# Optimization experiments

Hardware: AMD Instinct MI355X
Metric: run time of the kernel (lower is better)

Reference implementation:

```python
import jax, jax.numpy as jnp
import numpy as np

N_EMBD = 1024
N_HEAD = 16
LORA_R = 8
LORA_ALPHA = 16
SCALE = LORA_ALPHA / LORA_R


def lora_linear(x, W, b, A, Bm):
    # loralib: F.linear(x, W, b) + (x @ A.T @ B.T) * scaling
    return x @ W.T + b + ((x @ A.T) @ Bm.T) * SCALE


def setup_inputs() -> dict:
    key = jax.random.key(0)
    ks = jax.random.split(key, 9)
    B, T, C = 4, 2048, N_EMBD
    s_in = 1.0 / np.sqrt(C)
    x = jax.random.normal(ks[0], (B, T, C), dtype=jnp.float32)
    Wqkv = jax.random.normal(ks[1], (3 * C, C), dtype=jnp.float32) * s_in
    bqkv = jnp.zeros((3 * C,), dtype=jnp.float32)
    Aqkv = jax.random.normal(ks[2], (LORA_R, C), dtype=jnp.float32) * s_in
    Bqkv = jnp.zeros((3 * C, LORA_R), dtype=jnp.float32)  # loralib inits B to zero
    Wproj = jax.random.normal(ks[3], (C, C), dtype=jnp.float32) * s_in
    bproj = jnp.zeros((C,), dtype=jnp.float32)
    Aproj = jax.random.normal(ks[4], (LORA_R, C), dtype=jnp.float32) * s_in
    Bproj = jnp.zeros((C, LORA_R), dtype=jnp.float32)
    return {"x": x, "Wqkv": Wqkv, "bqkv": bqkv, "Aqkv": Aqkv, "Bqkv": Bqkv,
            "Wproj": Wproj, "bproj": bproj, "Aproj": Aproj, "Bproj": Bproj}


def reference(x, Wqkv, bqkv, Aqkv, Bqkv, Wproj, bproj, Aproj, Bproj):
    B, T, C = x.shape
    H, D = N_HEAD, C // N_HEAD
    qkv = lora_linear(x, Wqkv, bqkv, Aqkv, Bqkv)  # [B,T,3C]
    q, k, v = jnp.split(qkv, 3, axis=2)
    # [B,T,C] -> [B,H,T,D]
    q = q.reshape(B, T, H, D).transpose(0, 2, 1, 3)
    k = k.reshape(B, T, H, D).transpose(0, 2, 1, 3)
    v = v.reshape(B, T, H, D).transpose(0, 2, 1, 3)
    att = jnp.einsum("bhqd,bhkd->bhqk", q, k) * (1.0 / np.sqrt(D))
    causal = jnp.tril(jnp.ones((T, T), dtype=bool))
    att = jnp.where(causal[None, None], att, jnp.float32(-jnp.inf))
    att = jax.nn.softmax(att, axis=-1)
    out = jnp.einsum("bhqk,bhkd->bhqd", att, v)  # [B,H,T,D]
    out = out.transpose(0, 2, 1, 3).reshape(B, T, C)
    return lora_linear(out, Wproj, bproj, Aproj, Bproj)
```

## Files before the change

### kernel.cpp

```cpp
#include <hip/hip_runtime.h>
#include <hip/hip_bf16.h>

typedef __bf16 bf16_t;
typedef __bf16 bf16x8 __attribute__((ext_vector_type(8)));
typedef __bf16 bf16x4 __attribute__((ext_vector_type(4)));
typedef float  f32x4  __attribute__((ext_vector_type(4)));

#define MFMA_BF16 __builtin_amdgcn_mfma_f32_16x16x32_bf16
#define NEG_BIG  (-3.0e38f)

#if __has_builtin(__builtin_amdgcn_exp2f)
#define EXP2F(x) __builtin_amdgcn_exp2f(x)
#else
#define EXP2F(x) exp2f(x)
#endif

#define SBAR()       __builtin_amdgcn_s_barrier()
#define SCHED0()     __builtin_amdgcn_sched_barrier(0)
#define WAIT_LGKM0() asm volatile("s_waitcnt lgkmcnt(0)" ::: "memory")
#define WAIT_LGKM8() asm volatile("s_waitcnt lgkmcnt(8)" ::: "memory")
#define WAIT_VM0()   asm volatile("s_waitcnt vmcnt(0)" ::: "memory")
#define WAIT_VM4()   asm volatile("s_waitcnt vmcnt(4)" ::: "memory")
#define WAIT_VM6()   asm volatile("s_waitcnt vmcnt(6)" ::: "memory")

__device__ __forceinline__ void load16_lds(const bf16_t* g, bf16_t* l) {
    __builtin_amdgcn_global_load_lds(
        (const __attribute__((address_space(1))) void*)g,
        (__attribute__((address_space(3))) void*)l, 16, 0, 0);
}

__device__ inline bf16x8 ld8(const bf16_t* p) { return *(const bf16x8*)p; }
__device__ inline bf16x8 ld8(const float* p) {
    f32x4 a = *(const f32x4*)p;
    f32x4 b = *(const f32x4*)(p + 4);
    bf16x8 o;
    o[0] = (bf16_t)a[0]; o[1] = (bf16_t)a[1]; o[2] = (bf16_t)a[2]; o[3] = (bf16_t)a[3];
    o[4] = (bf16_t)b[0]; o[5] = (bf16_t)b[1]; o[6] = (bf16_t)b[2]; o[7] = (bf16_t)b[3];
    return o;
}

template <typename TX>
__device__ __forceinline__ void lora_xa_body(
    const TX* __restrict__ X, const float* __restrict__ A,
    float* __restrict__ out, int m, int lane)
{
    const TX* xp = X + (size_t)m * 1024;
    float acc[8];
#pragma unroll
    for (int r = 0; r < 8; r++) acc[r] = 0.f;

#pragma unroll 4
    for (int ci = 0; ci < 16; ci++) {
        int k = ci * 64 + lane;
        float xv = (float)xp[k];
#pragma unroll
        for (int r = 0; r < 8; r++) acc[r] += xv * A[r * 1024 + k];
    }
#pragma unroll
    for (int r = 0; r < 8; r++) {
        float v = acc[r];
        v += __shfl_xor(v, 1);  v += __shfl_xor(v, 2);  v += __shfl_xor(v, 4);
        v += __shfl_xor(v, 8);  v += __shfl_xor(v, 16); v += __shfl_xor(v, 32);
        if (lane == 0) out[m * 8 + r] = v;
    }
}

template <typename TX>
__global__ __launch_bounds__(256) void lora_xa_kernel(
    const TX* __restrict__ X, const float* __restrict__ A,
    float* __restrict__ out)
{
    const int lane = threadIdx.x & 63;
    const int w    = threadIdx.x >> 6;
    const int m    = blockIdx.x * 4 + w;
    lora_xa_body<TX>(X, A, out, m, lane);
}

__global__ __launch_bounds__(256) void prep_kernel(
    const float* __restrict__ x, const float* __restrict__ Wqkv,
    const float* __restrict__ Wproj,
    bf16_t* __restrict__ x16, bf16_t* __restrict__ Wqkv16,
    bf16_t* __restrict__ Wproj16,
    const float* __restrict__ Aqkv, float* __restrict__ xa1)
{
    const int bid = blockIdx.x;
    if (bid < 6144) {
        const float* in; bf16_t* out; size_t off;
        if (bid < 4096)      { in = x;     out = x16;     off = (size_t)bid * 2048; }
        else if (bid < 5632) { in = Wqkv;  out = Wqkv16;  off = (size_t)(bid - 4096) * 2048; }
        else                 { in = Wproj; out = Wproj16; off = (size_t)(bid - 5632) * 2048; }
        size_t i = off + (size_t)threadIdx.x * 8;
        *(bf16x8*)&out[i] = ld8(&in[i]);
    } else {
        const int lane = threadIdx.x & 63;
        const int w    = threadIdx.x >> 6;
        const int m    = (bid - 6144) * 4 + w;
        lora_xa_body<float>(x, Aqkv, xa1, m, lane);
    }
}

__device__ __forceinline__ void gemm_epilogue(
    f32x4 (&acc)[4][4], const float* bias, const float* xA, const float* LB,
    bf16_t* C0, bf16_t* C1, bf16_t* C2, float* Cf,
    int tile_m, int tile_n, int wm, int wn, int c, int g)
{
    const int seg    = tile_n >> 10;
    const int tn_loc = tile_n & 1023;
    bf16_t* Cout = (seg == 0) ? C0 : (seg == 1) ? C1 : C2;

    float biasf[4];
    float lbv[4][8];
#pragma unroll
    for (int j = 0; j < 4; j++) {
        int col = tile_n + wn + j * 16 + c;
        biasf[j] = bias[col];
        f32x4 lb0 = *(const f32x4*)&LB[(size_t)col * 8];
        f32x4 lb1 = *(const f32x4*)&LB[(size_t)col * 8 + 4];
#pragma unroll
        for (int r = 0; r < 4; r++) { lbv[j][r] = lb0[r]; lbv[j][r + 4] = lb1[r]; }
    }
#pragma unroll
    for (int i = 0; i < 4; i++) {
#pragma unroll
        for (int rg = 0; rg < 4; rg++) {
            int row = tile_m + wm + i * 16 + g * 4 + rg;
            f32x4 xa0 = *(const f32x4*)&xA[(size_t)row * 8];
            f32x4 xa1 = *(const f32x4*)&xA[(size_t)row * 8 + 4];
#pragma unroll
            for (int j = 0; j < 4; j++) {
                float lora = xa0[0] * lbv[j][0] + xa0[1] * lbv[j][1] +
                             xa0[2] * lbv[j][2] + xa0[3] * lbv[j][3] +
                             xa1[0] * lbv[j][4] + xa1[1] * lbv[j][5] +
                             xa1[2] * lbv[j][6] + xa1[3] * lbv[j][7];
                float v = acc[i][j][rg] + biasf[j] + 2.0f * lora;
                int lcol = tn_loc + wn + j * 16 + c;
                if (Cf) Cf[(size_t)row * 1024 + lcol] = v;
                else    Cout[(size_t)row * 1024 + lcol] = (bf16_t)v;
            }
        }
    }
}

template <typename TA, typename TW>
__global__ __launch_bounds__(256) void gemm_bias_lora(
    const TA* __restrict__ A, const TW* __restrict__ W,
    const float* __restrict__ bias, const float* __restrict__ xA,
    const float* __restrict__ LB,
    bf16_t* __restrict__ C0, bf16_t* __restrict__ C1, bf16_t* __restrict__ C2,
    float* __restrict__ Cf, int K)
{
    __shared__ __align__(16) bf16_t As[128 * 72];
    __shared__ __align__(16) bf16_t Bs[128 * 72];

    const int t    = threadIdx.x;
    const int lane = t & 63;
    const int w    = t >> 6;
    const int wm   = (w >> 1) * 64;
    const int wn   = (w & 1) * 64;
    const int c    = lane & 15;
    const int g    = lane >> 4;
    const int tile_m = blockIdx.y * 128;
    const int tile_n = blockIdx.x * 128;

    const int srow = t >> 3;
    const int scol = (t & 7) * 8;

    f32x4 acc[4][4];
#pragma unroll
    for (int i = 0; i < 4; i++)
#pragma unroll
        for (int j = 0; j < 4; j++) {
            f32x4 z = {0.f, 0.f, 0.f, 0.f};
            acc[i][j] = z;
        }

    for (int k0 = 0; k0 < K; k0 += 64) {
#pragma unroll
        for (int i = 0; i < 4; i++) {
            int r = srow + i * 32;
            *(bf16x8*)&As[r * 72 + scol] = ld8(&A[(size_t)(tile_m + r) * K + k0 + scol]);
            *(bf16x8*)&Bs[r * 72 + scol] = ld8(&W[(size_t)(tile_n + r) * K + k0 + scol]);
        }
        __syncthreads();

#pragma unroll
        for (int kk = 0; kk < 2; kk++) {
            bf16x8 af[4], bfr[4];
#pragma unroll
            for (int i = 0; i < 4; i++)
                af[i] = *(const bf16x8*)&As[(wm + i * 16 + c) * 72 + kk * 32 + g * 8];
#pragma unroll
            for (int j = 0; j < 4; j++)
                bfr[j] = *(const bf16x8*)&Bs[(wn + j * 16 + c) * 72 + kk * 32 + g * 8];
#pragma unroll
            for (int i = 0; i < 4; i++)
#pragma unroll
                for (int j = 0; j < 4; j++)
                    acc[i][j] = MFMA_BF16(af[i], bfr[j], acc[i][j], 0, 0, 0);
        }
        __syncthreads();
    }
    gemm_epilogue(acc, bias, xA, LB, C0, C1, C2, Cf, tile_m, tile_n, wm, wn, c, g);
}

__global__ __launch_bounds__(512, 2) void gemm_256(
    const bf16_t* __restrict__ A, const bf16_t* __restrict__ W,
    const float* __restrict__ bias, const float* __restrict__ xA,
    const float* __restrict__ LB,
    bf16_t* __restrict__ C0, bf16_t* __restrict__ C1, bf16_t* __restrict__ C2,
    float* __restrict__ Cf, int K, int ntn)
{
    __shared__ __align__(16) bf16_t As[4][8192];
    __shared__ __align__(16) bf16_t Bs[4][8192];

    const int t    = threadIdx.x;
    const int lane = t & 63;
    const int w    = t >> 6;
    const int c    = lane & 15;
    const int g    = lane >> 4;

    const int nwg = gridDim.x;
    const int cpx = nwg >> 3;
    const int bid = blockIdx.x;
    const int swz = (bid & 7) * cpx + (bid >> 3);
    const int tile_m = (swz / ntn) * 256;
    const int tile_n = (swz % ntn) * 256;

    const int wm  = (w >> 2) * 128;
    const int wn  = (w & 3) * 64;
    const int ha  = w >> 2;
    const int hb  = wn >> 7;
    const int wnl = wn & 127;

    int aoffs[8][2], boffs[4][2];
#pragma unroll
    for (int il = 0; il < 8; il++) {
        int rl = il * 16 + c;
#pragma unroll
        for (int ks = 0; ks < 2; ks++)
            aoffs[il][ks] = rl * 64 + (((ks * 4 + g) ^ (rl & 7)) * 8);
    }
#pragma unroll
    for (int j2 = 0; j2 < 4; j2++) {
        int rl = wnl + j2 * 16 + c;
#pragma unroll
        for (int ks = 0; ks < 2; ks++)
            boffs[j2][ks] = rl * 64 + (((ks * 4 + g) ^ (rl & 7)) * 8);
    }

    const int trow = t >> 3;
    const int qq   = (t & 7) ^ (trow & 7);
    const bf16_t* aO = A + (size_t)(tile_m + trow) * K + qq * 8;
    const bf16_t* wO = W + (size_t)(tile_n + trow) * K + qq * 8;
    const size_t rK64 = (size_t)64 * K;

#define STAGE_A(T, h) do {                                                         \
    load16_lds(aO + (size_t)(h) * 128 * K + (size_t)(T) * 64,                      \
               &As[((T) & 1) * 2 + (h)][t * 8]);                                   \
    load16_lds(aO + (size_t)(h) * 128 * K + rK64 + (size_t)(T) * 64,               \
               &As[((T) & 1) * 2 + (h)][4096 + t * 8]); } while (0)
#define STAGE_B(T, h) do {                                                         \
    load16_lds(wO + (size_t)(h) * 128 * K + (size_t)(T) * 64,                      \
               &Bs[((T) & 1) * 2 + (h)][t * 8]);                                   \
    load16_lds(wO + (size_t)(h) * 128 * K + rK64 + (size_t)(T) * 64,               \
               &Bs[((T) & 1) * 2 + (h)][4096 + t * 8]); } while (0)

    f32x4 acc[8][4];
#pragma unroll
    for (int i = 0; i < 8; i++)
#pragma unroll
        for (int j2 = 0; j2 < 4; j2++) {
            f32x4 z = {0.f, 0.f, 0.f, 0.f};
            acc[i][j2] = z;
        }

    const int NT = K >> 6;

    STAGE_B(0, 0); STAGE_B(0, 1); STAGE_A(0, 0); STAGE_A(0, 1);
    WAIT_VM4();
    STAGE_B(1, 0); STAGE_B(1, 1); STAGE_A(1, 0);
    WAIT_VM6();
    SBAR();

    for (int j = 0; j < NT; j++) {
        const bf16_t* Ab = &As[(j & 1) * 2 + ha][0];
        const bf16_t* Bb = &Bs[(j & 1) * 2 + hb][0];
        bf16x8 bfr[4][2], af0[4], af1[4];

#pragma unroll
        for (int j2 = 0; j2 < 4; j2++) {
            bfr[j2][0] = *(const bf16x8*)&Bb[boffs[j2][0]];
            bfr[j2][1] = *(const bf16x8*)&Bb[boffs[j2][1]];
        }
#pragma unroll
        for (int i = 0; i < 4; i++) af0[i] = *(const bf16x8*)&Ab[aoffs[i][0]];
        if (j + 1 < NT) STAGE_A(j + 1, 1);
        WAIT_LGKM8();
        SBAR();
        WAIT_LGKM0();
        SCHED0();
        __builtin_amdgcn_s_setprio(1);
#pragma unroll
        for (int i = 0; i < 4; i++)
#pragma unroll
            for (int j2 = 0; j2 < 4; j2++)
                acc[i][j2] = MFMA_BF16(af0[i], bfr[j2][0], acc[i][j2], 0, 0, 0);
        __builtin_amdgcn_s_setprio(0);
        SBAR();

#pragma unroll
        for (int i = 0; i < 4; i++) af1[i] = *(const bf16x8*)&Ab[aoffs[i + 4][0]];
        if (j + 2 < NT) STAGE_B(j + 2, 0);
        SBAR();
        WAIT_LGKM0();
        SCHED0();
        __builtin_amdgcn_s_setprio(1);
#pragma unroll
        for (int i = 0; i < 4; i++)
#pragma unroll
            for (int j2 = 0; j2 < 4; j2++)
                acc[4 + i][j2] = MFMA_BF16(af1[i], bfr[j2][0], acc[4 + i][j2], 0, 0, 0);
        __builtin_amdgcn_s_setprio(0);
        SBAR();

#pragma unroll
        for (int i = 0; i < 4; i++) af0[i] = *(const bf16x8*)&Ab[aoffs[i][1]];
#pragma unroll
        for (int i = 0; i < 4; i++) af1[i] = *(const bf16x8*)&Ab[aoffs[i + 4][1]];
        if (j + 2 < NT) STAGE_B(j + 2, 1);
        SBAR();
        WAIT_LGKM0();
        SCHED0();
        __builtin_amdgcn_s_setprio(1);
#pragma unroll
        for (int i = 0; i < 4; i++)
#pragma unroll
            for (int j2 = 0; j2 < 4; j2++)
                acc[i][j2] = MFMA_BF16(af0[i], bfr[j2][1], acc[i][j2], 0, 0, 0);
        __builtin_amdgcn_s_setprio(0);
        SBAR();

        if (j + 2 < NT) STAGE_A(j + 2, 0);
        SBAR();
        __builtin_amdgcn_s_setprio(1);
#pragma unroll
        for (int i = 0; i < 4; i++)
#pragma unroll
            for (int j2 = 0; j2 < 4; j2++)
                acc[4 + i][j2] = MFMA_BF16(af1[i], bfr[j2][1], acc[4 + i][j2], 0, 0, 0);
        __builtin_amdgcn_s_setprio(0);
        if (j < NT - 2) WAIT_VM6(); else WAIT_VM0();
        SBAR();
    }
#undef STAGE_A
#undef STAGE_B

    const int seg    = tile_n >> 10;
    const int tn_loc = tile_n & 1023;
    bf16_t* Cout = (seg == 0) ? C0 : (seg == 1) ? C1 : C2;

    float biasf[4];
    float lbv[4][8];
#pragma unroll
    for (int j2 = 0; j2 < 4; j2++) {
        int col = tile_n + wn + j2 * 16 + c;
        biasf[j2] = bias[col];
        f32x4 lb0 = *(const f32x4*)&LB[(size_t)col * 8];
        f32x4 lb1 = *(const f32x4*)&LB[(size_t)col * 8 + 4];
#pragma unroll
        for (int r = 0; r < 4; r++) { lbv[j2][r] = lb0[r]; lbv[j2][r + 4] = lb1[r]; }
    }
#pragma unroll
    for (int i = 0; i < 8; i++) {
#pragma unroll
        for (int rg = 0; rg < 4; rg++) {
            int row = tile_m + wm + i * 16 + g * 4 + rg;
            f32x4 xa0 = *(const f32x4*)&xA[(size_t)row * 8];
            f32x4 xa1 = *(const f32x4*)&xA[(size_t)row * 8 + 4];
#pragma unroll
            for (int j2 = 0; j2 < 4; j2++) {
                float lora = xa0[0] * lbv[j2][0] + xa0[1] * lbv[j2][1] +
                             xa0[2] * lbv[j2][2] + xa0[3] * lbv[j2][3] +
                             xa1[0] * lbv[j2][4] + xa1[1] * lbv[j2][5] +
                             xa1[2] * lbv[j2][6] + xa1[3] * lbv[j2][7];
                float v = acc[i][j2][rg] + biasf[j2] + 2.0f * lora;
                int lcol = tn_loc + wn + j2 * 16 + c;
                if (Cf) Cf[(size_t)row * 1024 + lcol] = v;
                else    Cout[(size_t)row * 1024 + lcol] = (bf16_t)v;
            }
        }
    }
}

#define VT_IDX(d, kv) ((d) * 72 + ((d) >> 4) * 8 + (kv))
#define PS_IDX(q, kv) ((q) * 72 + ((q) >> 2) * 8 + (kv))
#define PW_REGION 1168

__global__ __launch_bounds__(256, 4) void attn_kernel(
    bf16_t* __restrict__ Q, const bf16_t* __restrict__ Kg,
    const bf16_t* __restrict__ Vg)
{
    __shared__ __align__(16) bf16_t Ks[64 * 72];
    __shared__ __align__(16) bf16_t Vt[64 * 72 + 32];
    __shared__ __align__(16) bf16_t Ps[4 * PW_REGION];

    const int t    = threadIdx.x;
    const int lane = t & 63;
    const int w    = t >> 6;
    const int c    = lane & 15;
    const int g    = lane >> 4;

    const int id = blockIdx.x;
    const int qb = 31 - (id >> 6);
    const int h  = id & 15;
    const int b  = (id >> 4) & 3;
    const int q0 = qb * 64;
    const size_t base = (size_t)b * 2048 * 1024;

    bf16x8 qf[2];
    {
        int qrow = q0 + w * 16 + c;
        const bf16_t* qp = Q + base + (size_t)qrow * 1024 + h * 64;
        qf[0] = *(const bf16x8*)&qp[g * 8];
        qf[1] = *(const bf16x8*)&qp[32 + g * 8];
    }

    bf16x8 ones;
#pragma unroll
    for (int e = 0; e < 8; e++) ones[e] = (bf16_t)1.0f;

    f32x4 acc_o[4];
#pragma unroll
    for (int jd = 0; jd < 4; jd++) {
        f32x4 z = {0.f, 0.f, 0.f, 0.f};
        acc_o[jd] = z;
    }
    f32x4 acc_l = {0.f, 0.f, 0.f, 0.f};
    float m_run = NEG_BIG;

    const int sr = t >> 2;
    const int sc = (t & 3) * 16;
    const int vtbase = VT_IDX(sc, sr);

    bf16x8 kr0, kr1, vr0, vr1;
    {
        const bf16_t* kp = Kg + base + (size_t)sr * 1024 + h * 64 + sc;
        kr0 = *(const bf16x8*)&kp[0];
        kr1 = *(const bf16x8*)&kp[8];
        const bf16_t* vp = Vg + base + (size_t)sr * 1024 + h * 64 + sc;
        vr0 = *(const bf16x8*)&vp[0];
        vr1 = *(const bf16x8*)&vp[8];
    }

    for (int kt = 0; kt <= qb; kt++) {
        if (kt > 0) __syncthreads();
        *(bf16x8*)&Ks[sr * 72 + sc]     = kr0;
        *(bf16x8*)&Ks[sr * 72 + sc + 8] = kr1;
#pragma unroll
        for (int e = 0; e < 8; e++) Vt[vtbase + e * 72]       = vr0[e];
#pragma unroll
        for (int e = 0; e < 8; e++) Vt[vtbase + (e + 8) * 72] = vr1[e];
        __syncthreads();

        if (kt < qb) {
            const bf16_t* kp = Kg + base + (size_t)((kt + 1) * 64 + sr) * 1024 + h * 64 + sc;
            kr0 = *(const bf16x8*)&kp[0];
            kr1 = *(const bf16x8*)&kp[8];
            const bf16_t* vp = Vg + base + (size_t)((kt + 1) * 64 + sr) * 1024 + h * 64 + sc;
            vr0 = *(const bf16x8*)&vp[0];
            vr1 = *(const bf16x8*)&vp[8];
        }

        f32x4 s[4];
#pragma unroll
        for (int j = 0; j < 4; j++) {
            f32x4 z = {0.f, 0.f, 0.f, 0.f};
            s[j] = z;
        }
#pragma unroll
        for (int kk = 0; kk < 2; kk++) {
            bf16x8 kf[4];
#pragma unroll
            for (int j = 0; j < 4; j++)
                kf[j] = *(const bf16x8*)&Ks[(j * 16 + c) * 72 + kk * 32 + g * 8];
#pragma unroll
            for (int j = 0; j < 4; j++)
                s[j] = MFMA_BF16(kf[j], qf[kk], s[j], 0, 0, 0);
        }

        const float SCL = 0.125f * 1.44269504088896f;
#pragma unroll
        for (int j = 0; j < 4; j++)
#pragma unroll
            for (int r = 0; r < 4; r++) s[j][r] *= SCL;

        if (kt == qb) {
#pragma unroll
            for (int j = 0; j < 4; j++)
#pragma unroll
                for (int r = 0; r < 4; r++)
                    if (j * 16 + g * 4 + r > w * 16 + c) s[j][r] = NEG_BIG;
        }

        float mx;
        {
            float a0 = fmaxf(fmaxf(s[0][0], s[0][1]), fmaxf(s[0][2], s[0][3]));
            float a1 = fmaxf(fmaxf(s[1][0], s[1][1]), fmaxf(s[1][2], s[1][3]));
            float a2 = fmaxf(fmaxf(s[2][0], s[2][1]), fmaxf(s[2][2], s[2][3]));
            float a3 = fmaxf(fmaxf(s[3][0], s[3][1]), fmaxf(s[3][2], s[3][3]));
            mx = fmaxf(fmaxf(a0, a1), fmaxf(a2, a3));
            mx = fmaxf(mx, __shfl_xor(mx, 16));
            mx = fmaxf(mx, __shfl_xor(mx, 32));
        }

        if (!__all(mx <= m_run + 8.0f)) {
            float mnew  = fmaxf(m_run, mx);
            float alpha = EXP2F(m_run - mnew);
            m_run = mnew;
#pragma unroll
            for (int jd = 0; jd < 4; jd++)
#pragma unroll
                for (int r = 0; r < 4; r++) acc_o[jd][r] *= alpha;
            acc_l[0] *= alpha;
        }

#pragma unroll
        for (int j = 0; j < 4; j++)
#pragma unroll
            for (int r = 0; r < 4; r++) s[j][r] = EXP2F(s[j][r] - m_run);

        bf16_t* Pw = &Ps[w * PW_REGION];
#pragma unroll
        for (int j = 0; j < 4; j++) {
            bf16x4 pk;
#pragma unroll
            for (int r = 0; r < 4; r++) pk[r] = (bf16_t)s[j][r];
            *(bf16x4*)&Pw[PS_IDX(c, j * 16 + g * 4)] = pk;
        }

#pragma unroll
        for (int kkv = 0; kkv < 2; kkv++) {
            bf16x8 pf = *(const bf16x8*)&Pw[PS_IDX(c, kkv * 32 + g * 8)];
#pragma unroll
            for (int jd = 0; jd < 4; jd++) {
                bf16x8 vf = *(const bf16x8*)&Vt[VT_IDX(jd * 16 + c, kkv * 32 + g * 8)];
                acc_o[jd] = MFMA_BF16(vf, pf, acc_o[jd], 0, 0, 0);
            }
            acc_l = MFMA_BF16(ones, pf, acc_l, 0, 0, 0);
        }
    }

    float rl = 1.0f / acc_l[0];
    int qrow = q0 + w * 16 + c;
    bf16_t* op = Q + base + (size_t)qrow * 1024 + h * 64;
#pragma unroll
    for (int jd = 0; jd < 4; jd++) {
        bf16x4 o4;
#pragma unroll
        for (int r = 0; r < 4; r++) o4[r] = (bf16_t)(acc_o[jd][r] * rl);
        *(bf16x4*)&op[jd * 16 + g * 4] = o4;
    }
}

extern "C" void kernel_launch(void* const* d_in, const int* in_sizes, int n_in,
                              void* d_out, int out_size, void* d_ws, size_t ws_size,
                              hipStream_t stream) {
    const float* x     = (const float*)d_in[0];
    const float* Wqkv  = (const float*)d_in[1];
    const float* bqkv  = (const float*)d_in[2];
    const float* Aqkv  = (const float*)d_in[3];
    const float* Bqkv  = (const float*)d_in[4];
    const float* Wproj = (const float*)d_in[5];
    const float* bproj = (const float*)d_in[6];
    const float* Aproj = (const float*)d_in[7];
    const float* Bproj = (const float*)d_in[8];
    float* out = (float*)d_out;

    char* ws = (char*)d_ws;
    const bool big = ws_size >= (size_t)(72.5 * 1024 * 1024) + 65536;

    if (big) {
        float*  xa1    = (float*)ws;
        float*  xa2    = (float*)(ws + 262144);
        bf16_t* x16    = (bf16_t*)(ws + 524288);
        bf16_t* Wqkv16 = x16 + (size_t)8192 * 1024;
        bf16_t* Wproj16= Wqkv16 + (size_t)3072 * 1024;
        bf16_t* Qfull  = Wproj16 + (size_t)1024 * 1024;
        bf16_t* Kfull  = Qfull + (size_t)8192 * 1024;
        bf16_t* Vfull  = Kfull + (size_t)8192 * 1024;

        prep_kernel<<<8192, 256, 0, stream>>>(
            x, Wqkv, Wproj, x16, Wqkv16, Wproj16, Aqkv, xa1);

        gemm_256<<<384, 512, 0, stream>>>(
            x16, Wqkv16, bqkv, xa1, Bqkv, Qfull, Kfull, Vfull, nullptr, 1024, 12);

        attn_kernel<<<2048, 256, 0, stream>>>(Qfull, Kfull, Vfull);

        lora_xa_kernel<bf16_t><<<2048, 256, 0, stream>>>(Qfull, Aproj, xa2);

        gemm_256<<<128, 512, 0, stream>>>(
            Qfull, Wproj16, bproj, xa2, Bproj,
            nullptr, nullptr, nullptr, out, 1024, 4);
    } else {
        float*  xa1   = (float*)ws;
        float*  xa2   = (float*)(ws + 262144);
        bf16_t* Qfull = (bf16_t*)(ws + 524288);
        bf16_t* Kfull = Qfull + (size_t)8192 * 1024;
        bf16_t* Vfull = Kfull + (size_t)8192 * 1024;

        lora_xa_kernel<float><<<2048, 256, 0, stream>>>(x, Aqkv, xa1);
        gemm_bias_lora<float, float><<<dim3(24, 64), 256, 0, stream>>>(
            x, Wqkv, bqkv, xa1, Bqkv, Qfull, Kfull, Vfull, nullptr, 1024);
        attn_kernel<<<2048, 256, 0, stream>>>(Qfull, Kfull, Vfull);
        lora_xa_kernel<bf16_t><<<2048, 256, 0, stream>>>(Qfull, Aproj, xa2);
        gemm_bias_lora<bf16_t, float><<<dim3(8, 64), 256, 0, stream>>>(
            Qfull, Wproj, bproj, xa2, Bproj,
            nullptr, nullptr, nullptr, out, 1024);
    }
}
```

Measured before the change: 331.6 us.

## Process two query tiles per attention block and use async-LDS GEMM for projection

The attention kernel now gives each workgroup two 64-row query tiles that share every K/V tile staged in LDS. This halves the number of K/V loads and LDS transposes per query, at the cost of more registers and an occupancy hint lowered from 4 to 2. The output projection switches from gemm_256 to a new 128x128-tile GEMM that loads straight to LDS with an XOR swizzle and launches more workgroups. The new GEMM is single-buffered and has a barrier every K step, which may expose load latency.

Result: faster. 305.8 us (-7.8%).

```diff
diff --git a/kernel.cpp b/kernel.cpp
--- a/kernel.cpp
+++ b/kernel.cpp
@@ -203,6 +203,71 @@
     gemm_epilogue(acc, bias, xA, LB, C0, C1, C2, Cf, tile_m, tile_n, wm, wn, c, g);
 }
 
+#define AS_OFF(row, q) ((row) * 64 + (((q) ^ ((row) & 7)) * 8))
+
+__global__ __launch_bounds__(256) void gemm_async(
+    const bf16_t* __restrict__ A, const bf16_t* __restrict__ W,
+    const float* __restrict__ bias, const float* __restrict__ xA,
+    const float* __restrict__ LB,
+    bf16_t* __restrict__ C0, bf16_t* __restrict__ C1, bf16_t* __restrict__ C2,
+    float* __restrict__ Cf, int K)
+{
+    __shared__ __align__(16) bf16_t As[128 * 64];
+    __shared__ __align__(16) bf16_t Bs[128 * 64];
+
+    const int t    = threadIdx.x;
+    const int lane = t & 63;
+    const int w    = t >> 6;
+    const int wm   = (w >> 1) * 64;
+    const int wn   = (w & 1) * 64;
+    const int c    = lane & 15;
+    const int g    = lane >> 4;
+    const int tile_m = blockIdx.y * 128;
+    const int tile_n = blockIdx.x * 128;
+
+    const int trow = t >> 3;
+    const int k8   = (t & 7) ^ (trow & 7);
+    const bf16_t* Ab = A + (size_t)tile_m * K + k8 * 8;
+    const bf16_t* Wb = W + (size_t)tile_n * K + k8 * 8;
+
+    f32x4 acc[4][4];
+#pragma unroll
+    for (int i = 0; i < 4; i++)
+#pragma unroll
+        for (int j = 0; j < 4; j++) {
+            f32x4 z = {0.f, 0.f, 0.f, 0.f};
+            acc[i][j] = z;
+        }
+
+    for (int k0 = 0; k0 < K; k0 += 64) {
+#pragma unroll
+        for (int i = 0; i < 4; i++) {
+            int row = i * 32 + trow;
+            load16_lds(&Ab[(size_t)row * K + k0], &As[(i * 256 + t) * 8]);
+            load16_lds(&Wb[(size_t)row * K + k0], &Bs[(i * 256 + t) * 8]);
+        }
+        __syncthreads();
+
+#pragma unroll
+        for (int kk = 0; kk < 2; kk++) {
+            bf16x8 af[4], bfr[4];
+#pragma unroll
+            for (int i = 0; i < 4; i++)
+                af[i] = *(const bf16x8*)&As[AS_OFF(wm + i * 16 + c, kk * 4 + g)];
+#pragma unroll
+            for (int j = 0; j < 4; j++)
+                bfr[j] = *(const bf16x8*)&Bs[AS_OFF(wn + j * 16 + c, kk * 4 + g)];
+#pragma unroll
+            for (int i = 0; i < 4; i++)
+#pragma unroll
+                for (int j = 0; j < 4; j++)
+                    acc[i][j] = MFMA_BF16(af[i], bfr[j], acc[i][j], 0, 0, 0);
+        }
+        __syncthreads();
+    }
+    gemm_epilogue(acc, bias, xA, LB, C0, C1, C2, Cf, tile_m, tile_n, wm, wn, c, g);
+}
+
 __global__ __launch_bounds__(512, 2) void gemm_256(
     const bf16_t* __restrict__ A, const bf16_t* __restrict__ W,
     const float* __restrict__ bias, const float* __restrict__ xA,
@@ -396,13 +461,13 @@
 #define PS_IDX(q, kv) ((q) * 72 + ((q) >> 2) * 8 + (kv))
 #define PW_REGION 1168
 
-__global__ __launch_bounds__(256, 4) void attn_kernel(
+__global__ __launch_bounds__(256, 2) void attn_kernel(
     bf16_t* __restrict__ Q, const bf16_t* __restrict__ Kg,
     const bf16_t* __restrict__ Vg)
 {
     __shared__ __align__(16) bf16_t Ks[64 * 72];
     __shared__ __align__(16) bf16_t Vt[64 * 72 + 32];
-    __shared__ __align__(16) bf16_t Ps[4 * PW_REGION];
+    __shared__ __align__(16) bf16_t Ps[8 * PW_REGION];
 
     const int t    = threadIdx.x;
     const int lane = t & 63;
@@ -411,32 +476,36 @@
     const int g    = lane >> 4;
 
     const int id = blockIdx.x;
-    const int qb = 31 - (id >> 6);
+    const int qb = 15 - (id >> 6);
     const int h  = id & 15;
     const int b  = (id >> 4) & 3;
-    const int q0 = qb * 64;
+    const int q0 = qb * 128;
     const size_t base = (size_t)b * 2048 * 1024;
-
-    bf16x8 qf[2];
+    const int last = 2 * qb + 1;
+
+    bf16x8 qfA[2], qfB[2];
     {
-        int qrow = q0 + w * 16 + c;
-        const bf16_t* qp = Q + base + (size_t)qrow * 1024 + h * 64;
-        qf[0] = *(const bf16x8*)&qp[g * 8];
-        qf[1] = *(const bf16x8*)&qp[32 + g * 8];
+        const bf16_t* qpA = Q + base + (size_t)(q0 + w * 16 + c) * 1024 + h * 64;
+        qfA[0] = *(const bf16x8*)&qpA[g * 8];
+        qfA[1] = *(const bf16x8*)&qpA[32 + g * 8];
+        const bf16_t* qpB = qpA + (size_t)64 * 1024;
+        qfB[0] = *(const bf16x8*)&qpB[g * 8];
+        qfB[1] = *(const bf16x8*)&qpB[32 + g * 8];
     }
 
     bf16x8 ones;
 #pragma unroll
     for (int e = 0; e < 8; e++) ones[e] = (bf16_t)1.0f;
 
-    f32x4 acc_o[4];
+    f32x4 accA[4], accB[4];
 #pragma unroll
     for (int jd = 0; jd < 4; jd++) {
         f32x4 z = {0.f, 0.f, 0.f, 0.f};
-        acc_o[jd] = z;
-    }
-    f32x4 acc_l = {0.f, 0.f, 0.f, 0.f};
-    float m_run = NEG_BIG;
+        accA[jd] = z; accB[jd] = z;
+    }
+    f32x4 lA = {0.f, 0.f, 0.f, 0.f};
+    f32x4 lB = {0.f, 0.f, 0.f, 0.f};
+    float mA = NEG_BIG, mB = NEG_BIG;
 
     const int sr = t >> 2;
     const int sc = (t & 3) * 16;
@@ -452,7 +521,11 @@
         vr1 = *(const bf16x8*)&vp[8];
     }
 
-    for (int kt = 0; kt <= qb; kt++) {
+    bf16_t* PwA = &Ps[(w * 2 + 0) * PW_REGION];
+    bf16_t* PwB = &Ps[(w * 2 + 1) * PW_REGION];
+    const float SCL = 0.125f * 1.44269504088896f;
+
+    for (int kt = 0; kt <= last; kt++) {
         if (kt > 0) __syncthreads();
         *(bf16x8*)&Ks[sr * 72 + sc]     = kr0;
         *(bf16x8*)&Ks[sr * 72 + sc + 8] = kr1;
@@ -462,7 +535,7 @@
         for (int e = 0; e < 8; e++) Vt[vtbase + (e + 8) * 72] = vr1[e];
         __syncthreads();
 
-        if (kt < qb) {
+        if (kt < last) {
             const bf16_t* kp = Kg + base + (size_t)((kt + 1) * 64 + sr) * 1024 + h * 64 + sc;
             kr0 = *(const bf16x8*)&kp[0];
             kr1 = *(const bf16x8*)&kp[8];
@@ -471,11 +544,13 @@
             vr1 = *(const bf16x8*)&vp[8];
         }
 
-        f32x4 s[4];
+        const bool doA = (kt <= 2 * qb);
+
+        f32x4 sA[4], sB[4];
 #pragma unroll
         for (int j = 0; j < 4; j++) {
             f32x4 z = {0.f, 0.f, 0.f, 0.f};
-            s[j] = z;
+            sA[j] = z; sB[j] = z;
         }
 #pragma unroll
         for (int kk = 0; kk < 2; kk++) {
@@ -483,82 +558,148 @@
 #pragma unroll
             for (int j = 0; j < 4; j++)
                 kf[j] = *(const bf16x8*)&Ks[(j * 16 + c) * 72 + kk * 32 + g * 8];
+            if (doA) {
+#pragma unroll
+                for (int j = 0; j < 4; j++)
+                    sA[j] = MFMA_BF16(kf[j], qfA[kk], sA[j], 0, 0, 0);
+            }
 #pragma unroll
             for (int j = 0; j < 4; j++)
-                s[j] = MFMA_BF16(kf[j], qf[kk], s[j], 0, 0, 0);
-        }
-
-        const float SCL = 0.125f * 1.44269504088896f;
-#pragma unroll
-        for (int j = 0; j < 4; j++)
-#pragma unroll
-            for (int r = 0; r < 4; r++) s[j][r] *= SCL;
-
-        if (kt == qb) {
+                sB[j] = MFMA_BF16(kf[j], qfB[kk], sB[j], 0, 0, 0);
+        }
+
+        if (doA) {
 #pragma unroll
             for (int j = 0; j < 4; j++)
 #pragma unroll
-                for (int r = 0; r < 4; r++)
-                    if (j * 16 + g * 4 + r > w * 16 + c) s[j][r] = NEG_BIG;
-        }
-
-        float mx;
+                for (int r = 0; r < 4; r++) sA[j][r] *= SCL;
+            if (kt == 2 * qb) {
+#pragma unroll
+                for (int j = 0; j < 4; j++)
+#pragma unroll
+                    for (int r = 0; r < 4; r++)
+                        if (j * 16 + g * 4 + r > w * 16 + c) sA[j][r] = NEG_BIG;
+            }
+            float mx;
+            {
+                float a0 = fmaxf(fmaxf(sA[0][0], sA[0][1]), fmaxf(sA[0][2], sA[0][3]));
+                float a1 = fmaxf(fmaxf(sA[1][0], sA[1][1]), fmaxf(sA[1][2], sA[1][3]));
+                float a2 = fmaxf(fmaxf(sA[2][0], sA[2][1]), fmaxf(sA[2][2], sA[2][3]));
+                float a3 = fmaxf(fmaxf(sA[3][0], sA[3][1]), fmaxf(sA[3][2], sA[3][3]));
+                mx = fmaxf(fmaxf(a0, a1), fmaxf(a2, a3));
+                mx = fmaxf(mx, __shfl_xor(mx, 16));
+                mx = fmaxf(mx, __shfl_xor(mx, 32));
+            }
+            if (!__all(mx <= mA + 8.0f)) {
+                float mnew  = fmaxf(mA, mx);
+                float alpha = EXP2F(mA - mnew);
+                mA = mnew;
+#pragma unroll
+                for (int jd = 0; jd < 4; jd++)
+#pragma unroll
+                    for (int r = 0; r < 4; r++) accA[jd][r] *= alpha;
+                lA[0] *= alpha;
+            }
+#pragma unroll
+            for (int j = 0; j < 4; j++)
+#pragma unroll
+                for (int r = 0; r < 4; r++) sA[j][r] = EXP2F(sA[j][r] - mA);
+#pragma unroll
+            for (int j = 0; j < 4; j++) {
+                bf16x4 pk;
+#pragma unroll
+                for (int r = 0; r < 4; r++) pk[r] = (bf16_t)sA[j][r];
+                *(bf16x4*)&PwA[PS_IDX(c, j * 16 + g * 4)] = pk;
+            }
+        }
+
         {
-            float a0 = fmaxf(fmaxf(s[0][0], s[0][1]), fmaxf(s[0][2], s[0][3]));
-            float a1 = fmaxf(fmaxf(s[1][0], s[1][1]), fmaxf(s[1][2], s[1][3]));
-            float a2 = fmaxf(fmaxf(s[2][0], s[2][1]), fmaxf(s[2][2], s[2][3]));
-            float a3 = fmaxf(fmaxf(s[3][0], s[3][1]), fmaxf(s[3][2], s[3][3]));
-            mx = fmaxf(fmaxf(a0, a1), fmaxf(a2, a3));
-            mx = fmaxf(mx, __shfl_xor(mx, 16));
-            mx = fmaxf(mx, __shfl_xor(mx, 32));
-        }
-
-        if (!__all(mx <= m_run + 8.0f)) {
-            float mnew  = fmaxf(m_run, mx);
-            float alpha = EXP2F(m_run - mnew);
-            m_run = mnew;
+#pragma unroll
+            for (int j = 0; j < 4; j++)
+#pragma unroll
+                for (int r = 0; r < 4; r++) sB[j][r] *= SCL;
+            if (kt == last) {
+#pragma unroll
+                for (int j = 0; j < 4; j++)
+#pragma unroll
+                    for (int r = 0; r < 4; r++)
+                        if (j * 16 + g * 4 + r > w * 16 + c) sB[j][r] = NEG_BIG;
+            }
+            float mx;
+            {
+                float a0 = fmaxf(fmaxf(sB[0][0], sB[0][1]), fmaxf(sB[0][2], sB[0][3]));
+                float a1 = fmaxf(fmaxf(sB[1][0], sB[1][1]), fmaxf(sB[1][2], sB[1][3]));
+                float a2 = fmaxf(fmaxf(sB[2][0], sB[2][1]), fmaxf(sB[2][2], sB[2][3]));
+                float a3 = fmaxf(fmaxf(sB[3][0], sB[3][1]), fmaxf(sB[3][2], sB[3][3]));
+                mx = fmaxf(fmaxf(a0, a1), fmaxf(a2, a3));
+                mx = fmaxf(mx, __shfl_xor(mx, 16));
+                mx = fmaxf(mx, __shfl_xor(mx, 32));
+            }
+            if (!__all(mx <= mB + 8.0f)) {
+                float mnew  = fmaxf(mB, mx);
+                float alpha = EXP2F(mB - mnew);
+                mB = mnew;
+#pragma unroll
+                for (int jd = 0; jd < 4; jd++)
+#pragma unroll
+                    for (int r = 0; r < 4; r++) accB[jd][r] *= alpha;
+                lB[0] *= alpha;
+            }
+#pragma unroll
+            for (int j = 0; j < 4; j++)
+#pragma unroll
+                for (int r = 0; r < 4; r++) sB[j][r] = EXP2F(sB[j][r] - mB);
+#pragma unroll
+            for (int j = 0; j < 4; j++) {
+                bf16x4 pk;
+#pragma unroll
+                for (int r = 0; r < 4; r++) pk[r] = (bf16_t)sB[j][r];
+                *(bf16x4*)&PwB[PS_IDX(c, j * 16 + g * 4)] = pk;
+            }
+        }
+
+#pragma unroll
+        for (int kkv = 0; kkv < 2; kkv++) {
+            bf16x8 vf[4];
 #pragma unroll
             for (int jd = 0; jd < 4; jd++)
-#pragma unroll
-                for (int r = 0; r < 4; r++) acc_o[jd][r] *= alpha;
-            acc_l[0] *= alpha;
-        }
-
-#pragma unroll
-        for (int j = 0; j < 4; j++)
-#pragma unroll
-            for (int r = 0; r < 4; r++) s[j][r] = EXP2F(s[j][r] - m_run);
-
-        bf16_t* Pw = &Ps[w * PW_REGION];
-#pragma unroll
-        for (int j = 0; j < 4; j++) {
-            bf16x4 pk;
-#pragma unroll
-            for (int r = 0; r < 4; r++) pk[r] = (bf16_t)s[j][r];
-            *(bf16x4*)&Pw[PS_IDX(c, j * 16 + g * 4)] = pk;
-        }
-
-#pragma unroll
-        for (int kkv = 0; kkv < 2; kkv++) {
-            bf16x8 pf = *(const bf16x8*)&Pw[PS_IDX(c, kkv * 32 + g * 8)];
-#pragma unroll
-            for (int jd = 0; jd < 4; jd++) {
-                bf16x8 vf = *(const bf16x8*)&Vt[VT_IDX(jd * 16 + c, kkv * 32 + g * 8)];
-                acc_o[jd] = MFMA_BF16(vf, pf, acc_o[jd], 0, 0, 0);
-            }
-            acc_l = MFMA_BF16(ones, pf, acc_l, 0, 0, 0);
-        }
-    }
-
-    float rl = 1.0f / acc_l[0];
-    int qrow = q0 + w * 16 + c;
-    bf16_t* op = Q + base + (size_t)qrow * 1024 + h * 64;
-#pragma unroll
-    for (int jd = 0; jd < 4; jd++) {
-        bf16x4 o4;
-#pragma unroll
-        for (int r = 0; r < 4; r++) o4[r] = (bf16_t)(acc_o[jd][r] * rl);
-        *(bf16x4*)&op[jd * 16 + g * 4] = o4;
+                vf[jd] = *(const bf16x8*)&Vt[VT_IDX(jd * 16 + c, kkv * 32 + g * 8)];
+            if (doA) {
+                bf16x8 pfA = *(const bf16x8*)&PwA[PS_IDX(c, kkv * 32 + g * 8)];
+#pragma unroll
+                for (int jd = 0; jd < 4; jd++)
+                    accA[jd] = MFMA_BF16(vf[jd], pfA, accA[jd], 0, 0, 0);
+                lA = MFMA_BF16(ones, pfA, lA, 0, 0, 0);
+            }
+            bf16x8 pfB = *(const bf16x8*)&PwB[PS_IDX(c, kkv * 32 + g * 8)];
+#pragma unroll
+            for (int jd = 0; jd < 4; jd++)
+                accB[jd] = MFMA_BF16(vf[jd], pfB, accB[jd], 0, 0, 0);
+            lB = MFMA_BF16(ones, pfB, lB, 0, 0, 0);
+        }
+    }
+
+    {
+        float rl = 1.0f / lA[0];
+        bf16_t* op = Q + base + (size_t)(q0 + w * 16 + c) * 1024 + h * 64;
+#pragma unroll
+        for (int jd = 0; jd < 4; jd++) {
+            bf16x4 o4;
+#pragma unroll
+            for (int r = 0; r < 4; r++) o4[r] = (bf16_t)(accA[jd][r] * rl);
+            *(bf16x4*)&op[jd * 16 + g * 4] = o4;
+        }
+    }
+    {
+        float rl = 1.0f / lB[0];
+        bf16_t* op = Q + base + (size_t)(q0 + 64 + w * 16 + c) * 1024 + h * 64;
+#pragma unroll
+        for (int jd = 0; jd < 4; jd++) {
+            bf16x4 o4;
+#pragma unroll
+            for (int r = 0; r < 4; r++) o4[r] = (bf16_t)(accB[jd][r] * rl);
+            *(bf16x4*)&op[jd * 16 + g * 4] = o4;
+        }
     }
 }
 
@@ -595,13 +736,13 @@
         gemm_256<<<384, 512, 0, stream>>>(
             x16, Wqkv16, bqkv, xa1, Bqkv, Qfull, Kfull, Vfull, nullptr, 1024, 12);
 
-        attn_kernel<<<2048, 256, 0, stream>>>(Qfull, Kfull, Vfull);
+        attn_kernel<<<1024, 256, 0, stream>>>(Qfull, Kfull, Vfull);
 
         lora_xa_kernel<bf16_t><<<2048, 256, 0, stream>>>(Qfull, Aproj, xa2);
 
-        gemm_256<<<128, 512, 0, stream>>>(
+        gemm_async<<<dim3(8, 64), 256, 0, stream>>>(
             Qfull, Wproj16, bproj, xa2, Bproj,
-            nullptr, nullptr, nullptr, out, 1024, 4);
+            nullptr, nullptr, nullptr, out, 1024);
     } else {
         float*  xa1   = (float*)ws;
         float*  xa2   = (float*)(ws + 262144);
@@ -612,7 +753,7 @@
         lora_xa_kernel<float><<<2048, 256, 0, stream>>>(x, Aqkv, xa1);
         gemm_bias_lora<float, float><<<dim3(24, 64), 256, 0, stream>>>(
             x, Wqkv, bqkv, xa1, Bqkv, Qfull, Kfull, Vfull, nullptr, 1024);
-        attn_kernel<<<2048, 256, 0, stream>>>(Qfull, Kfull, Vfull);
+        attn_kernel<<<1024, 256, 0, stream>>>(Qfull, Kfull, Vfull);
         lora_xa_kernel<bf16_t><<<2048, 256, 0, stream>>>(Qfull, Aproj, xa2);
         gemm_bias_lora<bf16_t, float><<<dim3(8, 64), 256, 0, stream>>>(
             Qfull, Wproj, bproj, xa2, Bproj,
```
